# Kernel optimization log

Hardware: AMD Instinct MI355X
Metric: run time of the kernel (lower is better)

The kernel has to match this reference:

```python
import jax, jax.numpy as jnp
import numpy as np

B = 4096
INPUT_SIZE = 256
LATENT = 64
HIDDEN = 512
ACTIONS = 12
EXPERTS = 8
GATE_H = 128
IN_DIM = INPUT_SIZE + LATENT      # 320, first-layer expert in-dim
INTER = HIDDEN + LATENT           # 576, later-layer expert in-dim


def _lip_linear_params(key, out_f, in_f):
    kw, kb = jax.random.split(key)
    stdv = 1.0 / np.sqrt(in_f)
    W = jax.random.uniform(kw, (out_f, in_f), jnp.float32, -stdv, stdv)
    b = jax.random.uniform(kb, (out_f,), jnp.float32, -stdv, stdv)
    c = jnp.abs(W).sum(1).max()[None]  # shape (1,), matches init
    return W, b, c


def _expert_params(key, e, in_f, out_f):
    # kaiming_uniform_ on tensor of shape (E, in, out): fan_in computed by torch
    kw = key
    gain = np.sqrt(2.0)  # default a=sqrt(5) -> gain = sqrt(2/(1+5)) ... torch uses a=math.sqrt(5)? no: default a=0
    # torch.nn.init.kaiming_uniform_(weight) default a=0, fan_in = in*out? torch computes fan from dims[1:]
    fan_in = in_f
    bound = np.sqrt(6.0 / fan_in)
    W = jax.random.uniform(kw, (e, in_f, out_f), jnp.float32, -bound, bound)
    b = jnp.full((e, out_f), 0.01, jnp.float32)
    return W, b


def setup_inputs() -> dict:
    key = jax.random.key(0)
    ks = jax.random.split(key, 10)
    z = jax.random.normal(ks[0], (B, LATENT), jnp.float32)
    c = jax.random.normal(ks[1], (B, INPUT_SIZE), jnp.float32)
    w0, b0 = _expert_params(ks[2], EXPERTS, IN_DIM, HIDDEN)
    w1, b1 = _expert_params(ks[3], EXPERTS, INTER, HIDDEN)
    w2, b2 = _expert_params(ks[4], EXPERTS, INTER, ACTIONS)
    gw0, gb0, gc0 = _lip_linear_params(ks[5], GATE_H, IN_DIM)
    gw1, gb1, gc1 = _lip_linear_params(ks[6], GATE_H, GATE_H)
    gw2, gb2, gc2 = _lip_linear_params(ks[7], EXPERTS, GATE_H)
    return {"z": z, "c": c, "w0": w0, "b0": b0, "w1": w1, "b1": b1,
            "w2": w2, "b2": b2, "gw0": gw0, "gb0": gb0, "gc0": gc0,
            "gw1": gw1, "gb1": gb1, "gc1": gc1, "gw2": gw2, "gb2": gb2, "gc2": gc2}


def _lip_linear(x, W, b, cc):
    # LipschitzLinear: scale rows of W so row-wise L1 norm <= softplus(c)
    lipc = jax.nn.softplus(cc)                      # (1,)
    scale = jnp.minimum(lipc / jnp.abs(W).sum(1), 1.0)  # (out,)
    return x @ (W * scale[:, None]).T + b


def _moe_forward(z, c, coeff, layers):
    layer_out = c
    for W, bias, act in layers:
        inp = jnp.concatenate([z, layer_out], axis=1)       # (B, in)
        # per-expert GEMM then coefficient mix: avoids (B,in,out) intermediate
        h = jnp.einsum('bi,eio->beo', inp, W)               # (B, E, out)
        out = jnp.einsum('be,beo->bo', coeff, h) + coeff @ bias
        layer_out = jax.nn.elu(out) if act else out
    return layer_out


def reference(z, c, w0, b0, w1, b1, w2, b2,
              gw0, gb0, gc0, gw1, gb1, gc1, gw2, gb2, gc2):
    x = jnp.concatenate([z, c], axis=1)
    h = jax.nn.elu(_lip_linear(x, gw0, gb0, gc0))
    h = jax.nn.elu(_lip_linear(h, gw1, gb1, gc1))
    logits = _lip_linear(h, gw2, gb2, gc2)
    coeff = jax.nn.softmax(logits, axis=1)                  # (B, E)
    layers = [(w0, b0, True), (w1, b1, True), (w2, b2, False)]
    return _moe_forward(z, c, coeff, layers)
```

## Files before the change

kernel.cpp:

```cpp
#include <hip/hip_runtime.h>
#include <hip/hip_bf16.h>
#include <hip/hip_fp16.h>
#include <math.h>

#define BATCH 4096
#define INPUT_SIZE 256
#define LATENT 64
#define HIDDEN 512
#define ACTIONS 12
#define EXPERTS 8
#define GATE_H 128
#define IN_DIM (INPUT_SIZE + LATENT)
#define INTER (HIDDEN + LATENT)

typedef unsigned int u32;
typedef unsigned short u16;
typedef __attribute__((ext_vector_type(8))) short short8;
typedef __attribute__((ext_vector_type(8))) _Float16 f16x8;
typedef __attribute__((ext_vector_type(16))) float f32x16;

__device__ __forceinline__ u16 f2h(float x) { return __half_as_ushort(__float2half(x)); }
__device__ __forceinline__ float h2f(u16 u) { return __half2float(__ushort_as_half(u)); }

__device__ __forceinline__ void gload16(const void* g, void* lds) {
    __builtin_amdgcn_global_load_lds(
        (const __attribute__((address_space(1))) u32*)g,
        (__attribute__((address_space(3))) u32*)lds, 16, 0, 0);
}

#define GS 4
__global__ __launch_bounds__(256) void gate_forward_v4(
    const float* __restrict__ z, const float* __restrict__ c,
    const float* __restrict__ W0t, const float* __restrict__ b0,
    const float* __restrict__ W1t, const float* __restrict__ b1,
    const float* __restrict__ W2t, const float* __restrict__ b2,
    float* __restrict__ coeff) {
    __shared__ float xs[GS][IN_DIM + 2];
    __shared__ float hq[4][GS][GATE_H];
    __shared__ float h1[GS][GATE_H + 1];
    __shared__ float h2[GS][GATE_H + 1];
    __shared__ float red[GS][EXPERTS];

    const int b4 = blockIdx.x * GS;
    const int t = threadIdx.x;
    const int np = t & 63, kq = t >> 6;
    const int n0 = np * 2;

    for (int idx = t; idx < GS * IN_DIM; idx += 256) {
        const int s = idx / IN_DIM, i = idx - s * IN_DIM;
        xs[s][i] = (i < LATENT) ? z[(size_t)(b4 + s) * LATENT + i]
                                : c[(size_t)(b4 + s) * INPUT_SIZE + (i - LATENT)];
    }
    __syncthreads();

    {
        float a0[GS], a1[GS];
        #pragma unroll
        for (int s = 0; s < GS; ++s) { a0[s] = 0.f; a1[s] = 0.f; }
        const int i0 = kq * 80;
        #pragma unroll 8
        for (int i = i0; i < i0 + 80; ++i) {
            const float2 wv2 = *(const float2*)(W0t + (size_t)i * GATE_H + n0);
            #pragma unroll
            for (int s = 0; s < GS; ++s) {
                a0[s] = fmaf(xs[s][i], wv2.x, a0[s]);
                a1[s] = fmaf(xs[s][i], wv2.y, a1[s]);
            }
        }
        #pragma unroll
        for (int s = 0; s < GS; ++s) { hq[kq][s][n0] = a0[s]; hq[kq][s][n0 + 1] = a1[s]; }
    }
    __syncthreads();
    if (kq == 0) {
        #pragma unroll
        for (int s = 0; s < GS; ++s)
            #pragma unroll
            for (int j = 0; j < 2; ++j) {
                const int n = n0 + j;
                const float v = b0[n] + hq[0][s][n] + hq[1][s][n] + hq[2][s][n] + hq[3][s][n];
                h1[s][n] = v > 0.f ? v : expm1f(v);
            }
    }
    __syncthreads();

    {
        float a0[GS], a1[GS];
        #pragma unroll
        for (int s = 0; s < GS; ++s) { a0[s] = 0.f; a1[s] = 0.f; }
        const int i0 = kq * 32;
        #pragma unroll 8
        for (int i = i0; i < i0 + 32; ++i) {
            const float2 wv2 = *(const float2*)(W1t + (size_t)i * GATE_H + n0);
            #pragma unroll
            for (int s = 0; s < GS; ++s) {
                a0[s] = fmaf(h1[s][i], wv2.x, a0[s]);
                a1[s] = fmaf(h1[s][i], wv2.y, a1[s]);
            }
        }
        #pragma unroll
        for (int s = 0; s < GS; ++s) { hq[kq][s][n0] = a0[s]; hq[kq][s][n0 + 1] = a1[s]; }
    }
    __syncthreads();
    if (kq == 0) {
        #pragma unroll
        for (int s = 0; s < GS; ++s)
            #pragma unroll
            for (int j = 0; j < 2; ++j) {
                const int n = n0 + j;
                const float v = b1[n] + hq[0][s][n] + hq[1][s][n] + hq[2][s][n] + hq[3][s][n];
                h2[s][n] = v > 0.f ? v : expm1f(v);
            }
    }
    __syncthreads();

    if (t < GS * EXPERTS) {
        const int s = t >> 3, e = t & 7;
        float acc = b2[e];
        #pragma unroll 8
        for (int i = 0; i < GATE_H; ++i)
            acc = fmaf(h2[s][i], W2t[(size_t)i * EXPERTS + e], acc);
        red[s][e] = acc;
    }
    __syncthreads();
    if (t < GS) {
        float m = red[t][0];
        #pragma unroll
        for (int i = 1; i < EXPERTS; ++i) m = fmaxf(m, red[t][i]);
        float e[EXPERTS];
        float sum = 0.f;
        #pragma unroll
        for (int i = 0; i < EXPERTS; ++i) { e[i] = expf(red[t][i] - m); sum += e[i]; }
        const float inv = 1.f / sum;
        #pragma unroll
        for (int i = 0; i < EXPERTS; ++i)
            coeff[(size_t)(b4 + t) * EXPERTS + i] = e[i] * inv;
    }
}

__global__ __launch_bounds__(256) void pack_all_kernel(
    const float* __restrict__ w0, const float* __restrict__ w1,
    const float* __restrict__ w2,
    const float* __restrict__ z, const float* __restrict__ c,
    u16* __restrict__ Bpk0, u16* __restrict__ Bpk1, u16* __restrict__ Bpk2,
    u16* __restrict__ Apk0, u16* __restrict__ Apk1, u16* __restrict__ Apk2,
    const float* __restrict__ gw0, const float* __restrict__ gc0,
    const float* __restrict__ gw1, const float* __restrict__ gc1,
    const float* __restrict__ gw2, const float* __restrict__ gc2,
    float* __restrict__ gW0t, float* __restrict__ gW1t, float* __restrict__ gW2t) {
    const int t = threadIdx.x, wv = t >> 6, l = t & 63;
    const int x = blockIdx.x, y = blockIdx.y;

    if (y < 33) {
        __shared__ float tile[4][16][33];
        const float* w; u16* Bpk; int IN, OUT, nblk;
        if (y < 16)      { w = w0; Bpk = Bpk0; IN = IN_DIM; OUT = HIDDEN;  nblk = y; }
        else if (y < 32) { w = w1; Bpk = Bpk1; IN = INTER;  OUT = HIDDEN;  nblk = y - 16; }
        else             { w = w2; Bpk = Bpk2; IN = INTER;  OUT = ACTIONS; nblk = 0; }
        const int NK = IN / 16;
        const int e = x, n0 = nblk * 32;
        const int col = l & 31, half = l >> 5;
        char* base = (char*)Bpk + ((size_t)(nblk * EXPERTS + e) * NK) * 1024;

        for (int jj = wv; jj < NK; jj += 4) {
            #pragma unroll
            for (int i = 0; i < 8; ++i) {
                const int r = i * 2 + half;
                float v = 0.f;
                if (n0 + col < OUT) v = w[((size_t)e * IN + jj * 16 + r) * OUT + n0 + col];
                tile[wv][r][col] = v;
            }
            short8 hh;
            #pragma unroll
            for (int i = 0; i < 8; ++i)
                hh[i] = (short)f2h(tile[wv][half * 8 + i][col]);
            *(short8*)(base + (size_t)jj * 1024 + l * 16) = hh;
        }
    } else if (y < 49) {
        constexpr int NK0 = 20, NK1 = 36;
        const int bblk = (y - 33) * 8 + x;
        const int r = l & 31, half = l >> 5;
        const int row = bblk * 32 + r;
        char* base0 = (char*)Apk0 + (size_t)bblk * NK0 * 1024;
        char* base1 = (char*)Apk1 + (size_t)bblk * NK1 * 1024;
        char* base2 = (char*)Apk2 + (size_t)bblk * NK1 * 1024;

        for (int jj = wv; jj < NK0; jj += 4) {
            const int k = jj * 16 + half * 8;
            const float* src = (k < LATENT) ? (z + (size_t)row * LATENT + k)
                                            : (c + (size_t)row * INPUT_SIZE + (k - LATENT));
            short8 hh;
            #pragma unroll
            for (int i = 0; i < 8; ++i) hh[i] = (short)f2h(src[i]);
            *(short8*)(base0 + (size_t)jj * 1024 + l * 16) = hh;
            if (jj < 4) {
                *(short8*)(base1 + (size_t)jj * 1024 + l * 16) = hh;
                *(short8*)(base2 + (size_t)jj * 1024 + l * 16) = hh;
            }
        }
    } else {
        const int row_g = (y - 49) * 32 + x * 4 + wv;
        if (row_g < 264) {
            const float* W; const float* cc; float* Wt; int cols, rows, row;
            if (row_g < 128)      { W = gw0; cc = gc0; Wt = gW0t; cols = IN_DIM; rows = GATE_H; row = row_g; }
            else if (row_g < 256) { W = gw1; cc = gc1; Wt = gW1t; cols = GATE_H; rows = GATE_H; row = row_g - 128; }
            else                  { W = gw2; cc = gc2; Wt = gW2t; cols = GATE_H; rows = EXPERTS; row = row_g - 256; }
            const float* w = W + (size_t)row * cols;
            float s = 0.f;
            for (int i = l; i < cols; i += 64) s += fabsf(w[i]);
            #pragma unroll
            for (int off = 32; off > 0; off >>= 1) s += __shfl_down(s, off, 64);
            s = __shfl(s, 0, 64);
            const float cv = cc[0];
            const float lipc = (cv > 0.f) ? (cv + log1pf(expf(-cv))) : log1pf(expf(cv));
            const float scale = fminf(lipc / s, 1.0f);
            for (int i = l; i < cols; i += 64)
                Wt[(size_t)i * rows + row] = w[i] * scale;
        }
    }
}

template<int NPART>
__global__ __launch_bounds__(256) void reduce_pack_kernel(
    const u16* __restrict__ P16, const float* __restrict__ coeff,
    const float* __restrict__ bias, u16* __restrict__ ApkNext) {
    constexpr int NK = 36;
    __shared__ float biasS[EXPERTS][256];
    __shared__ float coeffS[32][9];
    const int t = threadIdx.x, wv = t >> 6, l = t & 63;
    const int bblk = blockIdx.x, ch = blockIdx.y;
    const int r = l & 31, half = l >> 5;
    const int row = bblk * 32 + r;

    for (int idx = t; idx < EXPERTS * 256; idx += 256)
        biasS[idx >> 8][idx & 255] = bias[(idx >> 8) * HIDDEN + ch * 256 + (idx & 255)];
    for (int idx = t; idx < 32 * 8; idx += 256)
        coeffS[idx >> 3][idx & 7] = coeff[(size_t)(bblk * 32 + (idx >> 3)) * 8 + (idx & 7)];
    __syncthreads();

    char* base = (char*)ApkNext + (size_t)bblk * NK * 1024;
    for (int jj = ch * 16 + wv; jj < ch * 16 + 16; jj += 4) {
        const int cb = jj * 16 + half * 8;
        float v[8];
        #pragma unroll
        for (int i = 0; i < 8; ++i) v[i] = 0.f;
        #pragma unroll
        for (int p = 0; p < NPART; ++p) {
            const short8 q = *(const short8*)(P16 + ((size_t)p * BATCH + row) * HIDDEN + cb);
            #pragma unroll
            for (int i = 0; i < 8; ++i) v[i] += h2f((u16)q[i]);
        }
        #pragma unroll
        for (int e = 0; e < EXPERTS; ++e) {
            const float cv = coeffS[r][e];
            #pragma unroll
            for (int i = 0; i < 8; ++i) v[i] = fmaf(cv, biasS[e][cb - ch * 256 + i], v[i]);
        }
        short8 hh;
        #pragma unroll
        for (int i = 0; i < 8; ++i) {
            const float hv = v[i] > 0.f ? v[i] : expm1f(v[i]);
            hh[i] = (short)f2h(hv);
        }
        *(short8*)(base + (size_t)(4 + jj) * 1024 + l * 16) = hh;
    }
}

__global__ __launch_bounds__(256) void reduce_out_kernel(
    const float* __restrict__ P2, const float* __restrict__ coeff,
    const float* __restrict__ b2, float* __restrict__ out) {
    const int t = threadIdx.x;
    const int bblk = blockIdx.x;
    for (int idx = t; idx < 32 * ACTIONS; idx += 256) {
        const int r = idx / ACTIONS, n = idx % ACTIONS;
        const int row = bblk * 32 + r;
        float s = 0.f;
        #pragma unroll
        for (int p = 0; p < 8; ++p) s += P2[((size_t)p * BATCH + row) * 32 + n];
        const float* cf = coeff + (size_t)row * 8;
        #pragma unroll
        for (int e = 0; e < 8; ++e) s = fmaf(cf[e], b2[e * ACTIONS + n], s);
        out[(size_t)row * ACTIONS + n] = s;
    }
}

template<int NK, int WN, int EPB, int OUTW, int GX, int GY, int GZ, bool F16P>
__global__ __launch_bounds__(128 * WN) void moe_gemm(
    const u16* __restrict__ Apk, const u16* __restrict__ Bpk,
    const float* __restrict__ coeff, void* __restrict__ Pout) {
    constexpr int TOT = NK / 4;
    constexpr int NWAVE = 2 * WN;
    constexpr int CPW = 16 / NWAVE;
    constexpr int CPX = GX / 8;

    __shared__ __align__(16) char As[3 * 16384];
    __shared__ float coeffT[EPB][128];

    const int t = threadIdx.x, wv = t >> 6, l = t & 63;
    const int wr = wv & 1, wc = wv >> 1;

    const int fid = blockIdx.x + GX * (blockIdx.y + GY * blockIdx.z);
    const int xcd = fid & 7, idx = fid >> 3;
    const int bx = xcd * CPX + (idx % CPX);
    const int yz = idx / CPX;
    const int by = yz % GY, bz = yz / GY;

    const int b0 = bx * 128;
    const int bblk0 = bx * 4;
    const int nblkg = by * WN + wc;
    const int part = bz;
    const int estart = part * EPB;

    for (int idx2 = t; idx2 < EPB * 128; idx2 += 128 * WN)
        coeffT[idx2 >> 7][idx2 & 127] =
            coeff[(size_t)(b0 + (idx2 & 127)) * EXPERTS + estart + (idx2 >> 7)];

    const char* Ab = (const char*)Apk;
    const char* Bbase[EPB];
    #pragma unroll
    for (int e = 0; e < EPB; ++e)
        Bbase[e] = (const char*)Bpk +
                   ((size_t)(nblkg * EXPERTS + estart + e) * NK) * 1024 + l * 16;

    f32x16 accE[EPB][2];
    #pragma unroll
    for (int e = 0; e < EPB; ++e) { accE[e][0] = (f32x16)0.f; accE[e][1] = (f32x16)0.f; }

    f16x8 breg[2][EPB][4];

    auto stageA = [&](int s) {
        char* dst = As + (s % 3) * 16384;
        #pragma unroll
        for (int q = 0; q < CPW; ++q) {
            const int cf = wv * CPW + q, bb = cf >> 2, kq = cf & 3;
            gload16(Ab + ((size_t)(bblk0 + bb) * NK + s * 4 + kq) * 1024 + l * 16,
                    dst + cf * 1024 + l * 16);
        }
    };

    __syncthreads();

    stageA(0);
    #pragma unroll
    for (int e = 0; e < EPB; ++e)
        #pragma unroll
        for (int q = 0; q < 4; ++q)
            breg[0][e][q] = *(const f16x8*)(Bbase[e] + (size_t)q * 1024);
    stageA(1);
    #pragma unroll
    for (int e = 0; e < EPB; ++e)
        #pragma unroll
        for (int q = 0; q < 4; ++q)
            breg[1][e][q] = *(const f16x8*)(Bbase[e] + (size_t)(4 + q) * 1024);

    #pragma unroll
    for (int s = 0; s < TOT; ++s) {
        if (s == TOT - 1) asm volatile("s_waitcnt vmcnt(0)" ::: "memory");
        else              asm volatile("s_waitcnt vmcnt(12)" ::: "memory");
        __builtin_amdgcn_sched_barrier(0);
        __builtin_amdgcn_s_barrier();
        __builtin_amdgcn_sched_barrier(0);

        if (s + 2 < TOT) stageA(s + 2);

        const char* buf = As + (s % 3) * 16384;
        f16x8 af0[4], af1[4];
        #pragma unroll
        for (int j = 0; j < 4; ++j) {
            af0[j] = *(const f16x8*)(buf + ((wr * 2 + 0) * 4 + j) * 1024 + l * 16);
            af1[j] = *(const f16x8*)(buf + ((wr * 2 + 1) * 4 + j) * 1024 + l * 16);
        }
        #pragma unroll
        for (int e = 0; e < EPB; ++e)
            #pragma unroll
            for (int j = 0; j < 4; ++j) {
                accE[e][0] = __builtin_amdgcn_mfma_f32_32x32x16_f16(af0[j], breg[s & 1][e][j], accE[e][0], 0, 0, 0);
                accE[e][1] = __builtin_amdgcn_mfma_f32_32x32x16_f16(af1[j], breg[s & 1][e][j], accE[e][1], 0, 0, 0);
            }
        if (s + 2 < TOT) {
            #pragma unroll
            for (int e = 0; e < EPB; ++e)
                #pragma unroll
                for (int q = 0; q < 4; ++q)
                    breg[s & 1][e][q] = *(const f16x8*)(Bbase[e] + (size_t)((s + 2) * 4 + q) * 1024);
        }
    }

    const int ncol = nblkg * 32 + (l & 31);
    #pragma unroll
    for (int m = 0; m < 2; ++m) {
        #pragma unroll
        for (int g = 0; g < 16; ++g) {
            const int rloc = (g & 3) + 8 * (g >> 2) + 4 * (l >> 5);
            const int row = wr * 64 + m * 32 + rloc;
            float v = 0.f;
            #pragma unroll
            for (int e = 0; e < EPB; ++e) v = fmaf(coeffT[e][row], accE[e][m][g], v);
            const size_t off = ((size_t)part * BATCH + b0 + row) * OUTW + ncol;
            if (F16P) ((u16*)Pout)[off] = f2h(v);
            else      ((float*)Pout)[off] = v;
        }
    }
}

extern "C" void kernel_launch(void* const* d_in, const int* in_sizes, int n_in,
                              void* d_out, int out_size, void* d_ws, size_t ws_size,
                              hipStream_t stream) {
    const float* z   = (const float*)d_in[0];
    const float* c   = (const float*)d_in[1];
    const float* w0  = (const float*)d_in[2];
    const float* b0  = (const float*)d_in[3];
    const float* w1  = (const float*)d_in[4];
    const float* b1  = (const float*)d_in[5];
    const float* w2  = (const float*)d_in[6];
    const float* b2  = (const float*)d_in[7];
    const float* gw0 = (const float*)d_in[8];
    const float* gb0 = (const float*)d_in[9];
    const float* gc0 = (const float*)d_in[10];
    const float* gw1 = (const float*)d_in[11];
    const float* gb1 = (const float*)d_in[12];
    const float* gc1 = (const float*)d_in[13];
    const float* gw2 = (const float*)d_in[14];
    const float* gb2 = (const float*)d_in[15];
    const float* gc2 = (const float*)d_in[16];
    float* out = (float*)d_out;

    char* p = (char*)d_ws;
    float* coeff = (float*)p;  p += (size_t)BATCH * EXPERTS * 4;
    float* gW0t  = (float*)p;  p += (size_t)GATE_H * IN_DIM * 4;
    float* gW1t  = (float*)p;  p += (size_t)GATE_H * GATE_H * 4;
    float* gW2t  = (float*)p;  p += (size_t)EXPERTS * GATE_H * 4;
    u16* Apk0 = (u16*)p;       p += (size_t)128 * 20 * 1024;
    u16* Apk1 = (u16*)p;       p += (size_t)128 * 36 * 1024;
    u16* Apk2 = (u16*)p;       p += (size_t)128 * 36 * 1024;
    u16* Bpk0 = (u16*)p;       p += (size_t)16 * 8 * 20 * 1024;
    u16* Bpk1 = (u16*)p;       p += (size_t)16 * 8 * 36 * 1024;
    u16* Bpk2 = (u16*)p;       p += (size_t)8 * 36 * 1024;
    u16* P16  = (u16*)p;       p += (size_t)4 * BATCH * HIDDEN * 2;
    float* P32 = (float*)P16;

    pack_all_kernel<<<dim3(8, 58), 256, 0, stream>>>(
        w0, w1, w2, z, c, Bpk0, Bpk1, Bpk2, Apk0, Apk1, Apk2,
        gw0, gc0, gw1, gc1, gw2, gc2, gW0t, gW1t, gW2t);

    gate_forward_v4<<<BATCH / GS, 256, 0, stream>>>(z, c, gW0t, gb0, gW1t, gb1,
                                                    gW2t, gb2, coeff);

    moe_gemm<20, 2, 2, HIDDEN, 32, 8, 4, true><<<dim3(32, 8, 4), 256, 0, stream>>>(
        Apk0, Bpk0, coeff, P16);
    reduce_pack_kernel<4><<<dim3(128, 2), 256, 0, stream>>>(P16, coeff, b0, Apk1);

    moe_gemm<36, 2, 2, HIDDEN, 32, 8, 4, true><<<dim3(32, 8, 4), 256, 0, stream>>>(
        Apk1, Bpk1, coeff, P16);
    reduce_pack_kernel<4><<<dim3(128, 2), 256, 0, stream>>>(P16, coeff, b1, Apk2);

    moe_gemm<36, 1, 1, 32, 32, 1, 8, false><<<dim3(32, 1, 8), 128, 0, stream>>>(
        Apk2, Bpk2, coeff, P32);
    reduce_out_kernel<<<128, 256, 0, stream>>>(P32, coeff, b2, out);
}
```

Measured before the change: 116.0 us.

## Use 512-thread MoE GEMM blocks with wider N tile sharing staged A

Adds a moe_gemm_big kernel in which each 8-wave block covers 128 rows by 128 columns, so one LDS-staged A tile is reused by twice as many output columns. The first two expert layers launch half as many blocks at twice the thread count. The goal is to halve the A-tile global loads and LDS staging per output, with an XCD-aware block remapping for locality. The cost is fewer blocks and more registers per block, which may reduce occupancy and latency hiding.

```diff
diff --git a/kernel.cpp b/kernel.cpp
--- a/kernel.cpp
+++ b/kernel.cpp
@@ -280,6 +280,120 @@
         #pragma unroll
         for (int e = 0; e < 8; ++e) s = fmaf(cf[e], b2[e * ACTIONS + n], s);
         out[(size_t)row * ACTIONS + n] = s;
+    }
+}
+
+template<int NK, bool F16P>
+__global__ __launch_bounds__(512) void moe_gemm_big(
+    const u16* __restrict__ Apk, const u16* __restrict__ Bpk,
+    const float* __restrict__ coeff, void* __restrict__ Pout) {
+    constexpr int TOT = NK / 4;
+
+    __shared__ __align__(16) char As[3 * 16384];
+    __shared__ float coeffT[2][128];
+
+    const int t = threadIdx.x, wv = t >> 6, l = t & 63;
+    const int wr = wv & 1, wc = wv >> 1;
+
+    const int fid = blockIdx.x + 32 * (blockIdx.y + 4 * blockIdx.z);
+    const int xcd = fid & 7, idx = fid >> 3;
+    const int bx = xcd * 4 + (idx & 3);
+    const int yz = idx >> 2;
+    const int by = yz & 3, bz = yz >> 2;
+
+    const int b0 = bx * 128;
+    const int bblk0 = bx * 4;
+    const int nblkg = by * 4 + wc;
+    const int part = bz;
+    const int estart = part * 2;
+
+    for (int i2 = t; i2 < 2 * 128; i2 += 512)
+        coeffT[i2 >> 7][i2 & 127] =
+            coeff[(size_t)(b0 + (i2 & 127)) * EXPERTS + estart + (i2 >> 7)];
+
+    const char* Ab = (const char*)Apk;
+    const char* Bbase[2];
+    #pragma unroll
+    for (int e = 0; e < 2; ++e)
+        Bbase[e] = (const char*)Bpk +
+                   ((size_t)(nblkg * EXPERTS + estart + e) * NK) * 1024 + l * 16;
+
+    f32x16 accE[2][2];
+    accE[0][0] = (f32x16)0.f; accE[0][1] = (f32x16)0.f;
+    accE[1][0] = (f32x16)0.f; accE[1][1] = (f32x16)0.f;
+
+    f16x8 breg[2][2][4];
+
+    auto stageA = [&](int s) {
+        char* dst = As + (s % 3) * 16384;
+        #pragma unroll
+        for (int q = 0; q < 2; ++q) {
+            const int cf = wv * 2 + q, bb = cf >> 2, kq = cf & 3;
+            gload16(Ab + ((size_t)(bblk0 + bb) * NK + s * 4 + kq) * 1024 + l * 16,
+                    dst + cf * 1024 + l * 16);
+        }
+    };
+
+    __syncthreads();
+
+    stageA(0);
+    #pragma unroll
+    for (int e = 0; e < 2; ++e)
+        #pragma unroll
+        for (int q = 0; q < 4; ++q)
+            breg[0][e][q] = *(const f16x8*)(Bbase[e] + (size_t)q * 1024);
+    stageA(1);
+    #pragma unroll
+    for (int e = 0; e < 2; ++e)
+        #pragma unroll
+        for (int q = 0; q < 4; ++q)
+            breg[1][e][q] = *(const f16x8*)(Bbase[e] + (size_t)(4 + q) * 1024);
+
+    #pragma unroll
+    for (int s = 0; s < TOT; ++s) {
+        if (s == TOT - 1) asm volatile("s_waitcnt vmcnt(0)" ::: "memory");
+        else              asm volatile("s_waitcnt vmcnt(10)" ::: "memory");
+        __builtin_amdgcn_sched_barrier(0);
+        __builtin_amdgcn_s_barrier();
+        __builtin_amdgcn_sched_barrier(0);
+
+        if (s + 2 < TOT) stageA(s + 2);
+
+        const char* buf = As + (s % 3) * 16384;
+        f16x8 af0[4], af1[4];
+        #pragma unroll
+        for (int j = 0; j < 4; ++j) {
+            af0[j] = *(const f16x8*)(buf + ((wr * 2 + 0) * 4 + j) * 1024 + l * 16);
+            af1[j] = *(const f16x8*)(buf + ((wr * 2 + 1) * 4 + j) * 1024 + l * 16);
+        }
+        #pragma unroll
+        for (int e = 0; e < 2; ++e)
+            #pragma unroll
+            for (int j = 0; j < 4; ++j) {
+                accE[e][0] = __builtin_amdgcn_mfma_f32_32x32x16_f16(af0[j], breg[s & 1][e][j], accE[e][0], 0, 0, 0);
+                accE[e][1] = __builtin_amdgcn_mfma_f32_32x32x16_f16(af1[j], breg[s & 1][e][j], accE[e][1], 0, 0, 0);
+            }
+        if (s + 2 < TOT) {
+            #pragma unroll
+            for (int e = 0; e < 2; ++e)
+                #pragma unroll
+                for (int q = 0; q < 4; ++q)
+                    breg[s & 1][e][q] = *(const f16x8*)(Bbase[e] + (size_t)((s + 2) * 4 + q) * 1024);
+        }
+    }
+
+    const int ncol = nblkg * 32 + (l & 31);
+    #pragma unroll
+    for (int m = 0; m < 2; ++m) {
+        #pragma unroll
+        for (int g = 0; g < 16; ++g) {
+            const int rloc = (g & 3) + 8 * (g >> 2) + 4 * (l >> 5);
+            const int row = wr * 64 + m * 32 + rloc;
+            float v = coeffT[0][row] * accE[0][m][g] + coeffT[1][row] * accE[1][m][g];
+            const size_t off = ((size_t)part * BATCH + b0 + row) * HIDDEN + ncol;
+            if (F16P) ((u16*)Pout)[off] = f2h(v);
+            else      ((float*)Pout)[off] = v;
+        }
     }
 }
 
@@ -445,11 +559,11 @@
     gate_forward_v4<<<BATCH / GS, 256, 0, stream>>>(z, c, gW0t, gb0, gW1t, gb1,
                                                     gW2t, gb2, coeff);
 
-    moe_gemm<20, 2, 2, HIDDEN, 32, 8, 4, true><<<dim3(32, 8, 4), 256, 0, stream>>>(
+    moe_gemm_big<20, true><<<dim3(32, 4, 4), 512, 0, stream>>>(
         Apk0, Bpk0, coeff, P16);
     reduce_pack_kernel<4><<<dim3(128, 2), 256, 0, stream>>>(P16, coeff, b0, Apk1);
 
-    moe_gemm<36, 2, 2, HIDDEN, 32, 8, 4, true><<<dim3(32, 8, 4), 256, 0, stream>>>(
+    moe_gemm_big<36, true><<<dim3(32, 4, 4), 512, 0, stream>>>(
         Apk1, Bpk1, coeff, P16);
     reduce_pack_kernel<4><<<dim3(128, 2), 256, 0, stream>>>(P16, coeff, b1, Apk2);
 
```

Measured after the change: 118.3 us. 1.02x slower.
